# Optimization experiments

Hardware: AMD Instinct MI355X
Metric: run time of the kernel (lower is better)

## Reference

```python
import jax, jax.numpy as jnp
import numpy as np

V = 50257      # vocab size
H = 512        # hidden size
S = 128        # source length
BEAM = 5       # beam width (matches beam_width=5 default)
TMAX = 32      # MAX_LENGTH decode cap
SOS, EOS = 1, 2
NEG = -1e9


def setup_inputs() -> dict:
    key = jax.random.key(0)
    ks = jax.random.split(key, 12)
    p = lambda k, shape: jax.random.normal(k, shape, jnp.float32) * 0.02
    return {
        "input_tokens": jax.random.randint(ks[0], (S,), 0, V),
        "embedding": p(ks[1], (V, H)),
        "enc_Wih": p(ks[2], (3 * H, H)),
        "enc_Whh": p(ks[3], (3 * H, H)),
        "enc_bih": jnp.zeros((3 * H,), jnp.float32),
        "enc_bhh": jnp.zeros((3 * H,), jnp.float32),
        "dec_Wih": p(ks[4], (3 * H, H)),
        "dec_Whh": p(ks[5], (3 * H, H)),
        "dec_bih": jnp.zeros((3 * H,), jnp.float32),
        "dec_bhh": jnp.zeros((3 * H,), jnp.float32),
        "W_concat": p(ks[6], (2 * H, H)),
        "W_vocab": p(ks[7], (H, V)),
    }


def gru_cell(x, h, Wih, Whh, bih, bhh):
    # x, h: [..., H]
    gi = x @ Wih.T + bih
    gh = h @ Whh.T + bhh
    ir, iz, inn = jnp.split(gi, 3, -1)
    hr, hz, hn = jnp.split(gh, 3, -1)
    r = jax.nn.sigmoid(ir + hr)
    z = jax.nn.sigmoid(iz + hz)
    n = jnp.tanh(inn + r * hn)
    return (1.0 - z) * n + z * h


def reference(input_tokens, embedding, enc_Wih, enc_Whh, enc_bih, enc_bhh,
              dec_Wih, dec_Whh, dec_bih, dec_bhh, W_concat, W_vocab):
    # ---- encoder: 1-layer GRU over source tokens ----
    src_emb = embedding[input_tokens]                       # [S, H]

    def enc_step(h, x):
        h2 = gru_cell(x, h, enc_Wih, enc_Whh, enc_bih, enc_bhh)
        return h2, h2

    enc_h, enc_out = jax.lax.scan(enc_step, jnp.zeros((H,), src_emb.dtype), src_emb)
    # enc_out: [S, H], enc_h: [H]

    def decode_step(tokens, hidden):
        # tokens: [B] int, hidden: [B, H]
        x = embedding[tokens]                               # [B, H]
        h = gru_cell(x, hidden, dec_Wih, dec_Whh, dec_bih, dec_bhh)
        attn = jax.nn.softmax(h @ enc_out.T, axis=-1)       # [B, S] Luong dot attention
        ctx = attn @ enc_out                                # [B, H]
        o = jnp.tanh(jnp.concatenate([h, ctx], -1) @ W_concat)
        logp = jax.nn.log_softmax(o @ W_vocab, axis=-1)     # [B, V]
        return logp, h

    # ---- batched beam search (GPU-resident equivalent of the heapq loop) ----
    tokens0 = jnp.full((BEAM,), SOS, jnp.int32)
    hidden0 = jnp.tile(enc_h[None], (BEAM, 1))
    scores0 = jnp.full((BEAM,), NEG, jnp.float32).at[0].set(0.0)
    fin0 = jnp.zeros((BEAM,), bool)
    len0 = jnp.ones((BEAM,), jnp.int32)
    seqs0 = jnp.zeros((BEAM, TMAX), jnp.int32)
    fin_row = jnp.full((V,), NEG, jnp.float32).at[EOS].set(0.0)

    def beam_step(state, t):
        tokens, hidden, scores, finished, lengths, seqs = state
        logp, h2 = decode_step(tokens, hidden)              # [BEAM, V]
        step_lp = jnp.where(finished[:, None], fin_row[None, :], logp)
        cand = scores[:, None] + step_lp                    # [BEAM, V]
        top_scores, flat = jax.lax.top_k(cand.reshape(-1), BEAM)
        parent = flat // V
        tok = (flat % V).astype(jnp.int32)
        par_fin = finished[parent]
        new_fin = par_fin | (tok == EOS)
        new_len = lengths[parent] + jnp.where(par_fin, 0, 1)
        new_seqs = seqs[parent].at[:, t].set(jnp.where(par_fin, 0, tok))
        return (tok, h2[parent], top_scores, new_fin, new_len, new_seqs), None

    state, _ = jax.lax.scan(beam_step, (tokens0, hidden0, scores0, fin0, len0, seqs0),
                            jnp.arange(TMAX))
    _, _, scores, _, lengths, seqs = state
    # length-normalized ranking, matching node.logp / node.leng sort
    norm = scores / lengths.astype(scores.dtype)
    order = jnp.argsort(-norm)
    return seqs[order], norm[order]
```

## Files before the change

### kernel.cpp

```cpp
#include <hip/hip_runtime.h>
#include <cstdint>
#include <cstddef>

#define V_SZ 50257
#define H_SZ 512
#define S_SZ 128
#define NBEAM 5
#define TMAXX 32
#define TOK_SOS 1
#define TOK_EOS 2
#define NEGINF (-1e9f)

#define GW 128
#define NT 512
#define GENC 16
#define COLS_PER_WG 393

#define BI_LEAF(l)  ((l)*32)
#define BI_ROOT     256
#define BI_REL(l)   (512 + (l)*32)
#define BI_ECNT     1024
#define BI_EREL     1056

#define OF_GI    0
#define OF_ENC   196608
#define OF_EW    262144
#define OF_H2    327680
#define OF_AL    332800
#define OF_OTOP  333440
#define OF_PV    336000
#define OF_PM    339200
#define OF_PS    339840
#define OF_SC    340480
#define OI_BASE  340488

template <typename T>
__device__ __forceinline__ T aload(const T* p){
  return __hip_atomic_load((T*)p, __ATOMIC_RELAXED, __HIP_MEMORY_SCOPE_AGENT);
}
template <typename T>
__device__ __forceinline__ void astore(T* p, T v){
  __hip_atomic_store(p, v, __ATOMIC_RELAXED, __HIP_MEMORY_SCOPE_AGENT);
}

__device__ __forceinline__ float wredsum(float a){
#pragma unroll
  for (int m = 32; m; m >>= 1) a += __shfl_xor(a, m, 64);
  return a;
}

template <typename F>
__device__ __forceinline__ void dbar(int* bi, int wid, F&& tail){
  __shared__ int s_last;
  int mygen = 0;
  __syncthreads();
  if (threadIdx.x == 0){
    int leaf = wid >> 4;
    mygen = aload(bi + BI_REL(leaf));
    __builtin_amdgcn_s_waitcnt(0);
    int lo = __hip_atomic_fetch_add(bi + BI_LEAF(leaf), 1, __ATOMIC_RELAXED, __HIP_MEMORY_SCOPE_AGENT);
    int last = 0;
    if (lo == 15){
      astore(bi + BI_LEAF(leaf), 0);
      __builtin_amdgcn_s_waitcnt(0);
      int ro = __hip_atomic_fetch_add(bi + BI_ROOT, 1, __ATOMIC_RELAXED, __HIP_MEMORY_SCOPE_AGENT);
      if (ro == (GW/16) - 1){
        astore(bi + BI_ROOT, 0);
        last = 1;
      }
    }
    if (!last){
      while (aload(bi + BI_REL(leaf)) == mygen) __builtin_amdgcn_s_sleep(4);
    }
    s_last = last;
  }
  __syncthreads();
  if (s_last){
    tail();
    __syncthreads();
    if (threadIdx.x == 0){
      __builtin_amdgcn_s_waitcnt(0);
#pragma unroll
      for (int l = 0; l < GW/16; ++l) astore(bi + BI_REL(l), mygen + 1);
    }
  }
  __syncthreads();
}

__global__ __launch_bounds__(256)
void k_gi(const int* __restrict__ toks, const float* __restrict__ emb,
          const float* __restrict__ eWih, const float* __restrict__ ebih,
          float* __restrict__ ws)
{
  float* fb = ws + 2048;
  float* gi = fb + OF_GI;
  const int tid = threadIdx.x, wid = blockIdx.x, lane = tid & 63, wvi = tid >> 6;
  int Wg = wid*4 + wvi;
  for (int it = 0; it < 192; ++it){
    int idx = Wg*192 + it;
    int s = idx / 1536, j = idx - s*1536;
    const float* er = emb + (size_t)toks[s]*H_SZ;
    const float* wr = eWih + (size_t)j*H_SZ;
    float a = 0.f;
#pragma unroll
    for (int u = 0; u < 8; ++u) a += er[u*64+lane]*wr[u*64+lane];
    a = wredsum(a);
    if (lane == 0) gi[idx] = a + ebih[j];
  }
  if (wid == 0){
    float* sc = fb + OF_SC;
    int* ib = (int*)(fb + OI_BASE);
    if (tid < NBEAM){
      sc[tid] = (tid==0) ? 0.f : NEGINF;
      ib[3200+tid] = TOK_SOS; ib[3208+tid] = 0; ib[3216+tid] = 1; ib[3224+tid] = 0;
    }
    for (int q = tid; q < 2*NBEAM*TMAXX; q += 256) ib[3232+q] = 0;
  }
}

__global__ __launch_bounds__(NT, 1)
void k_enc(const float* __restrict__ eWhh, const float* __restrict__ ebhh,
           float* __restrict__ ws)
{
  int* bi = (int*)ws;
  float* fb = ws + 2048;
  float* gi = fb + OF_GI;
  float* enc = fb + OF_ENC;
  const int tid = threadIdx.x, wid = blockIdx.x, lane = tid & 63, wvi = tid >> 6;
  const int i0 = wid*32;
  __shared__ float smF[96];

  float wreg[12][8];
#pragma unroll
  for (int dd = 0; dd < 12; ++dd){
    int d = wvi*12 + dd, g = d >> 5, il = d & 31;
    const float* wr = eWhh + (size_t)(g*512 + i0 + il)*H_SZ;
#pragma unroll
    for (int u = 0; u < 8; ++u) wreg[dd][u] = wr[u*64+lane];
  }

  for (int s = 0; s < S_SZ; ++s){
    float hreg[8];
    if (s == 0){
#pragma unroll
      for (int u = 0; u < 8; ++u) hreg[u] = 0.f;
    } else {
      const float* hp = enc + (size_t)(s-1)*H_SZ;
#pragma unroll
      for (int u = 0; u < 8; ++u) hreg[u] = aload(hp + u*64 + lane);
    }
#pragma unroll
    for (int dd = 0; dd < 12; ++dd){
      float a = 0.f;
#pragma unroll
      for (int u = 0; u < 8; ++u) a += wreg[dd][u]*hreg[u];
      a = wredsum(a);
      if (lane == 0) smF[wvi*12 + dd] = a;
    }
    __syncthreads();
    if (tid < 32){
      int i = i0 + tid;
      float gr = smF[tid], gz = smF[32+tid], gn = smF[64+tid];
      float gir = gi[s*1536 + i], giz = gi[s*1536 + 512 + i], gin = gi[s*1536 + 1024 + i];
      float hprev = (s==0) ? 0.f : aload(enc + (s-1)*H_SZ + i);
      float r = 1.f/(1.f + expf(-(gir + gr + ebhh[i])));
      float z = 1.f/(1.f + expf(-(giz + gz + ebhh[512+i])));
      float n = tanhf(gin + r*(gn + ebhh[1024+i]));
      astore(enc + s*H_SZ + i, (1.f - z)*n + z*hprev);
    }
    __syncthreads();
    if (tid == 0){
      int g = aload(bi + BI_EREL);
      __builtin_amdgcn_s_waitcnt(0);
      int lo = __hip_atomic_fetch_add(bi + BI_ECNT, 1, __ATOMIC_RELAXED, __HIP_MEMORY_SCOPE_AGENT);
      if (lo == GENC - 1){
        astore(bi + BI_ECNT, 0);
        __builtin_amdgcn_s_waitcnt(0);
        astore(bi + BI_EREL, g + 1);
      } else {
        while (aload(bi + BI_EREL) == g) __builtin_amdgcn_s_sleep(2);
      }
    }
    __syncthreads();
  }
}

__global__ __launch_bounds__(NT)
void k_ew(const float* __restrict__ Wc, float* __restrict__ ws)
{
  float* fb = ws + 2048;
  float* enc = fb + OF_ENC;
  float* EW  = fb + OF_EW;
  const int tid = threadIdx.x, wid = blockIdx.x;
  int jc = wid & 15, sb = wid >> 4;
  int jl = tid & 31, sl = (tid >> 5) & 15;
  int s = sb*16 + sl, j = jc*32 + jl;
  const float* er = enc + (size_t)s*H_SZ;
  const float* wc = Wc + (size_t)512*H_SZ;
  float a = 0.f;
  for (int k = 0; k < 512; ++k) a += er[k]*wc[(size_t)k*H_SZ + j];
  EW[s*H_SZ + j] = a;
}

__global__ __launch_bounds__(NT, 1)
void k_dec(const float* __restrict__ emb,
           const float* __restrict__ dWih, const float* __restrict__ dWhh,
           const float* __restrict__ dbih, const float* __restrict__ dbhh,
           const float* __restrict__ Wc,  const float* __restrict__ Wv,
           float* __restrict__ out, float* __restrict__ ws)
{
  const int wid = blockIdx.x, tid = threadIdx.x;
  const int lane = tid & 63, wvi = tid >> 6;
  int* bi = (int*)ws;
  float* fb = ws + 2048;
  float* enc  = fb + OF_ENC;
  float* EW   = fb + OF_EW;
  float* h2   = fb + OF_H2;
  float* al   = fb + OF_AL;
  float* otop = fb + OF_OTOP;
  float* pv   = fb + OF_PV;
  float* pm   = fb + OF_PM;
  float* ps   = fb + OF_PS;
  float* sc   = fb + OF_SC;
  int* ib   = (int*)(fb + OI_BASE);
  int* pidx = ib;
  int* tokA = ib + 3200;
  int* finA = ib + 3208;
  int* lenA = ib + 3216;
  int* parA = ib + 3224;
  int* seqA = ib + 3232;

  __shared__ float smF[1024];
  __shared__ int   smI[256];
  __shared__ float s_buf[2560];
  __shared__ float s_pp[648];

  for (int t = 0; t < TMAXX; ++t){
    float* h2new = h2 + (t & 1)*2560;
    float* h2old = h2 + ((t & 1) ^ 1)*2560;

    if (tid < NBEAM){ smI[tid] = aload(tokA + tid); smI[8 + tid] = t ? aload(parA + tid) : 0; }
    __syncthreads();
    if (t == 0){
      for (int q = tid; q < 2560; q += NT) s_buf[q] = enc[127*H_SZ + (q & 511)];
    } else {
      for (int q = tid; q < 2560; q += NT){
        int b = q >> 9;
        s_buf[q] = aload(h2old + smI[8 + b]*H_SZ + (q & 511));
      }
    }
    __syncthreads();
    {
      int i0 = wid*4;
      int mat = wvi >> 2;
      float srg[5][8];
      if (mat == 0){
#pragma unroll
        for (int b = 0; b < NBEAM; ++b){
          const float* sp = emb + (size_t)smI[b]*H_SZ;
#pragma unroll
          for (int u = 0; u < 8; ++u) srg[b][u] = sp[u*64+lane];
        }
      } else {
#pragma unroll
        for (int b = 0; b < NBEAM; ++b)
#pragma unroll
          for (int u = 0; u < 8; ++u) srg[b][u] = s_buf[b*512 + u*64 + lane];
      }
      for (int rr = 0; rr < 3; ++rr){
        int R = wvi*3 + rr;
        int rem = R - mat*12;
        int g = rem >> 2, il = rem & 3;
        const float* wr = ((mat==0) ? dWih : dWhh) + (size_t)(g*512 + i0 + il)*H_SZ;
        float wreg[8];
#pragma unroll
        for (int u = 0; u < 8; ++u) wreg[u] = wr[u*64+lane];
#pragma unroll
        for (int b = 0; b < NBEAM; ++b){
          float a = 0.f;
#pragma unroll
          for (int u = 0; u < 8; ++u) a += wreg[u]*srg[b][u];
          a = wredsum(a);
          if (lane == 0) smF[R*5 + b] = a;
        }
      }
      __syncthreads();
      if (tid < 20){
        int b = tid >> 2, il = tid & 3;
        int i = i0 + il;
        float ir  = smF[(0*12 + 0*4 + il)*5 + b] + dbih[i];
        float iz  = smF[(0*12 + 1*4 + il)*5 + b] + dbih[512+i];
        float inn = smF[(0*12 + 2*4 + il)*5 + b] + dbih[1024+i];
        float hr  = smF[(1*12 + 0*4 + il)*5 + b] + dbhh[i];
        float hz  = smF[(1*12 + 1*4 + il)*5 + b] + dbhh[512+i];
        float hn  = smF[(1*12 + 2*4 + il)*5 + b] + dbhh[1024+i];
        float r = 1.f/(1.f + expf(-(ir + hr)));
        float z = 1.f/(1.f + expf(-(iz + hz)));
        float n = tanhf(inn + r*hn);
        float hp = s_buf[b*512 + i];
        astore(h2new + b*H_SZ + i, (1.f - z)*n + z*hp);
      }
    }
    dbar(bi, wid, [&](){});

    for (int q = tid; q < 2560; q += NT) s_buf[q] = aload(h2new + q);
    __syncthreads();
    if (wvi < NBEAM){
      const float* er = enc + (size_t)wid*H_SZ;
      float a = 0.f;
#pragma unroll
      for (int u = 0; u < 8; ++u) a += er[u*64+lane]*s_buf[wvi*512 + u*64 + lane];
      a = wredsum(a);
      if (lane == 0) astore(al + wvi*S_SZ + wid, a);
    }
    if (tid < 320){
      int q = tid % 20, ksl = tid / 20;
      int f = wid*20 + q;
      int b = f >> 9, j = f & 511;
      float a = 0.f;
#pragma unroll 8
      for (int u = 0; u < 32; ++u){
        int k = ksl*32 + u;
        a += s_buf[b*512 + k]*Wc[(size_t)k*H_SZ + j];
      }
      smF[q*16 + ksl] = a;
    }
    __syncthreads();
    if (tid < 20){
      float a = 0.f;
#pragma unroll
      for (int u = 0; u < 16; ++u) a += smF[tid*16 + u];
      astore(otop + wid*20 + tid, a);
    }
    dbar(bi, wid, [&](){});

    if (wvi < NBEAM){
      float a1 = aload(al + wvi*S_SZ + lane), a2 = aload(al + wvi*S_SZ + 64 + lane);
      float m = fmaxf(a1, a2);
#pragma unroll
      for (int mm = 32; mm; mm >>= 1) m = fmaxf(m, __shfl_xor(m, mm, 64));
      float e1 = expf(a1 - m), e2 = expf(a2 - m);
      s_pp[wvi*128 + lane] = e1; s_pp[wvi*128 + 64 + lane] = e2;
      float ssv = wredsum(e1 + e2);
      if (lane == 0) s_pp[640 + wvi] = ssv;
    }
    __syncthreads();
    {
      float acc[5] = {0.f,0.f,0.f,0.f,0.f};
      for (int s2 = 0; s2 < 128; ++s2){
        float e = EW[(size_t)s2*H_SZ + tid];
#pragma unroll
        for (int b = 0; b < NBEAM; ++b) acc[b] += e*s_pp[b*128 + s2];
      }
#pragma unroll
      for (int b = 0; b < NBEAM; ++b)
        s_buf[b*512 + tid] = tanhf(aload(otop + b*512 + tid) + acc[b]/s_pp[640 + b]);
    }
    __syncthreads();
    {
      int vbase = wid*COLS_PER_WG;
      int v = vbase + tid;
      bool act = (tid < COLS_PER_WG) && (v < V_SZ);
      int vc = act ? v : vbase;
      const float* wp = Wv + vc;
      float a0=0.f,a1=0.f,a2=0.f,a3=0.f,a4=0.f;
      for (int hb = 0; hb < H_SZ; hb += 16){
        float wr[16];
#pragma unroll
        for (int u = 0; u < 16; ++u) wr[u] = wp[(size_t)(hb+u)*V_SZ];
#pragma unroll
        for (int u = 0; u < 16; ++u){
          float w = wr[u];
          a0 += w*s_buf[hb+u];
          a1 += w*s_buf[512+hb+u];
          a2 += w*s_buf[1024+hb+u];
          a3 += w*s_buf[1536+hb+u];
          a4 += w*s_buf[2048+hb+u];
        }
      }
      if (!act){ a0=a1=a2=a3=a4=-3e38f; }
      int myv = act ? v : 0x7FFFFFFF;
      float accs[5] = {a0,a1,a2,a3,a4};
#pragma unroll
      for (int b = 0; b < NBEAM; ++b){
        float x = accs[b];
        float m = x;
#pragma unroll
        for (int mm = 32; mm; mm >>= 1) m = fmaxf(m, __shfl_xor(m, mm, 64));
        float e = expf(x - m);
        float ssum = wredsum(e);
        float bv = x; int bc = myv;
        float w5[5]; int i5[5];
#pragma unroll
        for (int r = 0; r < 5; ++r){
          float cv2 = bv; int ci2 = bc;
#pragma unroll
          for (int mm = 32; mm; mm >>= 1){
            float ov = __shfl_xor(cv2, mm, 64); int oi = __shfl_xor(ci2, mm, 64);
            bool take = (ov > cv2) || (ov == cv2 && oi < ci2);
            cv2 = take ? ov : cv2; ci2 = take ? oi : ci2;
          }
          w5[r] = cv2; i5[r] = ci2;
          if (bc == ci2) bv = -3e38f;
        }
        if (lane == 0){
#pragma unroll
          for (int r = 0; r < 5; ++r){ smF[(wvi*5+b)*5+r] = w5[r]; smI[(wvi*5+b)*5+r] = i5[r]; }
          smF[300 + wvi*5 + b] = m;
          smF[360 + wvi*5 + b] = ssum;
        }
      }
      __syncthreads();
      if (tid < NBEAM){
        float M = -3.4e38f, Sv = 0.f;
#pragma unroll
        for (int w8 = 0; w8 < 8; ++w8){
          float m2 = smF[300 + w8*5 + tid], s2 = smF[360 + w8*5 + tid];
          if (m2 > M){ Sv = Sv*expf(M - m2) + s2; M = m2; }
          else       { Sv = Sv + s2*expf(m2 - M); }
        }
        astore(pm + wid*5 + tid, M); astore(ps + wid*5 + tid, Sv);
      }
      if (wvi < NBEAM){
        int b = wvi;
        float cval; int cidx;
        if (lane < 40){ cval = smF[((lane/5)*5 + b)*5 + (lane%5)]; cidx = smI[((lane/5)*5 + b)*5 + (lane%5)]; }
        else { cval = -3e38f; cidx = 0x7FFFFFFF; }
        float bv = cval; int bc = cidx;
#pragma unroll
        for (int r = 0; r < 5; ++r){
          float cv2 = bv; int ci2 = bc;
#pragma unroll
          for (int mm = 32; mm; mm >>= 1){
            float ov = __shfl_xor(cv2, mm, 64); int oi = __shfl_xor(ci2, mm, 64);
            bool take = (ov > cv2) || (ov == cv2 && oi < ci2);
            cv2 = take ? ov : cv2; ci2 = take ? oi : ci2;
          }
          if (lane == 0){ astore(pv + (wid*5+b)*5+r, cv2); astore(pidx + (wid*5+b)*5+r, ci2); }
          if (bc == ci2) bv = -3e38f;
        }
      }
    }
    dbar(bi, wid, [&](){
      int b5 = wvi;
      if (b5 < NBEAM){
        float m1 = aload(pm + lane*5 + b5), s1 = aload(ps + lane*5 + b5);
        float m2 = aload(pm + (64+lane)*5 + b5), s2 = aload(ps + (64+lane)*5 + b5);
        float M, Sv;
        if (m1 >= m2){ M = m1; Sv = s1 + s2*expf(m2 - m1); }
        else         { M = m2; Sv = s2 + s1*expf(m1 - m2); }
#pragma unroll
        for (int mm = 32; mm; mm >>= 1){
          float om = __shfl_xor(M, mm, 64), os = __shfl_xor(Sv, mm, 64);
          if (om > M){ Sv = Sv*expf(M - om) + os; M = om; }
          else       { Sv = Sv + os*expf(om - M); }
        }
        if (lane == 0){ smF[8 + b5] = M; smF[80 + b5] = logf(Sv); }
        float lv[5]; int li[5];
#pragma unroll
        for (int r = 0; r < 5; ++r){ lv[r] = aload(pv + (lane*5 + b5)*5 + r); li[r] = aload(pidx + (lane*5 + b5)*5 + r); }
        for (int r = 0; r < 5; ++r){
          float nv = aload(pv + ((64+lane)*5 + b5)*5 + r); int ni = aload(pidx + ((64+lane)*5 + b5)*5 + r);
          bool ins = (nv > lv[4]) || (nv == lv[4] && ni < li[4]);
          if (!ins) break;
          lv[4] = nv; li[4] = ni;
#pragma unroll
          for (int p = 4; p > 0; --p){
            bool sw = (lv[p] > lv[p-1]) || (lv[p] == lv[p-1] && li[p] < li[p-1]);
            if (sw){ float tv = lv[p]; lv[p] = lv[p-1]; lv[p-1] = tv;
                     int ti = li[p]; li[p] = li[p-1]; li[p-1] = ti; }
          }
        }
        float cv = lv[0]; int ci = li[0];
#pragma unroll
        for (int r = 0; r < 5; ++r){
          float xv = cv; int xi = ci;
#pragma unroll
          for (int mm = 32; mm; mm >>= 1){
            float ov = __shfl_xor(xv, mm, 64); int oi = __shfl_xor(xi, mm, 64);
            bool take = (ov > xv) || (ov == xv && oi < xi);
            xv = take ? ov : xv; xi = take ? oi : xi;
          }
          if (lane == 0){ smF[16 + b5*5 + r] = xv; smI[16 + b5*5 + r] = xi; }
          if (ci == xi){
            lv[0]=lv[1]; li[0]=li[1]; lv[1]=lv[2]; li[1]=li[2];
            lv[2]=lv[3]; li[2]=li[3]; lv[3]=lv[4]; li[3]=li[4];
            lv[4] = -3e38f; li[4] = 0x7FFFFFFF;
            cv = lv[0]; ci = li[0];
          }
        }
      }
      __syncthreads();
      if (wvi == 0){
        float cval = -3e38f; int cflat = 0x7FFFFFFF;
        int b = lane/5, k = lane - b*5;
        if (lane < 25){
          if (aload(finA + b)){
            if (k == 0){ cval = aload(sc + b) + 0.0f; cflat = b*V_SZ + TOK_EOS; }
          } else {
            cval = ((smF[16 + b*5 + k] - smF[8 + b]) - smF[80 + b]) + aload(sc + b);
            cflat = b*V_SZ + smI[16 + b*5 + k];
          }
        }
        float bv = cval; int bc = cflat;
#pragma unroll
        for (int r = 0; r < 5; ++r){
          float xv = bv; int xi = bc;
#pragma unroll
          for (int mm = 32; mm; mm >>= 1){
            float ov = __shfl_xor(xv, mm, 64); int oi = __shfl_xor(xi, mm, 64);
            bool take = (ov > xv) || (ov == xv && oi < xi);
            xv = take ? ov : xv; xi = take ? oi : xi;
          }
          if (lane == 0){ smF[48 + r] = xv; smI[48 + r] = xi; }
          if (bc == xi) bv = -3e38f;
        }
        if (lane < NBEAM){
          int r = lane;
          float nscore = smF[48 + r]; int nfl = smI[48 + r];
          int par = nfl / V_SZ; int tok = nfl - par*V_SZ;
          int ofin = aload(finA + par); int olen = aload(lenA + par);
          int nf = (ofin || tok == TOK_EOS) ? 1 : 0;
          int nl = olen + (ofin ? 0 : 1);
          astore(sc + r, nscore); astore(tokA + r, tok); astore(finA + r, nf);
          astore(lenA + r, nl); astore(parA + r, par);
          smI[56 + r] = par; smI[64 + r] = tok; smI[72 + r] = ofin; smI[80 + r] = nl;
          smF[56 + r] = nscore;
        }
      }
      __syncthreads();
      int cur = t & 1, nxt = 1 - cur;
      if (tid < 160){
        int r = tid >> 5, u = tid & 31;
        int par = smI[56 + r];
        int val = aload(seqA + cur*160 + par*32 + u);
        if (u == t) val = smI[72 + r] ? 0 : smI[64 + r];
        astore(seqA + nxt*160 + r*32 + u, val);
      }
      if (t == TMAXX - 1){
        __syncthreads();
        if (tid == 0){
          float nn[5];
#pragma unroll
          for (int r = 0; r < 5; ++r) nn[r] = smF[56 + r] / (float)smI[80 + r];
          int used = 0;
#pragma unroll
          for (int r = 0; r < 5; ++r){
            int best = -1;
            for (int q2 = 0; q2 < 5; ++q2){
              if (used & (1 << q2)) continue;
              if (best < 0 || nn[q2] > nn[best]) best = q2;
            }
            used |= (1 << best);
            smI[88 + r] = best; smF[64 + r] = nn[best];
          }
        }
        __syncthreads();
        if (tid < 160){
          int r = tid >> 5, u = tid & 31;
          int src = smI[88 + r];
          out[tid] = (float)aload(seqA + nxt*160 + src*32 + u);
        }
        if (tid >= 160 && tid < 165) out[tid] = smF[64 + (tid - 160)];
      }
    });
  }
}

extern "C" void kernel_launch(void* const* d_in, const int* in_sizes, int n_in,
                              void* d_out, int out_size, void* d_ws, size_t ws_size,
                              hipStream_t stream)
{
  (void)in_sizes; (void)n_in; (void)out_size; (void)ws_size;
  hipMemsetAsync(d_ws, 0, 8192, stream);
  float* ws = (float*)d_ws;
  k_gi<<<dim3(256), dim3(256), 0, stream>>>(
      (const int*)d_in[0], (const float*)d_in[1],
      (const float*)d_in[2], (const float*)d_in[4], ws);
  k_enc<<<dim3(GENC), dim3(NT), 0, stream>>>(
      (const float*)d_in[3], (const float*)d_in[5], ws);
  k_ew<<<dim3(128), dim3(NT), 0, stream>>>(
      (const float*)d_in[10], ws);
  k_dec<<<dim3(GW), dim3(NT), 0, stream>>>(
      (const float*)d_in[1],
      (const float*)d_in[6], (const float*)d_in[7],
      (const float*)d_in[8], (const float*)d_in[9],
      (const float*)d_in[10], (const float*)d_in[11],
      (float*)d_out, ws);
}
```

Baseline: 3.673 ms.

## Double decoder workgroups to 256 with split-K vocab projection and register-resident GRU weights

Raises the persistent decoder grid from 128 to 256 workgroups and allows two workgroups per CU. Each group now handles 197 vocab columns and splits the hidden dimension across two halves of the block, combining the halves through shared memory. GRU weight rows are preloaded into registers once, outside the time loop, and the attention and W_concat work and the cross-group top-k and softmax merges are redistributed for the larger grid. This spreads the memory-bound W_vocab streaming over more waves, at the cost of more participants in each grid barrier and an extra shared-memory reduction.

```diff
diff --git a/kernel.cpp b/kernel.cpp
--- a/kernel.cpp
+++ b/kernel.cpp
@@ -11,16 +11,16 @@
 #define TOK_EOS 2
 #define NEGINF (-1e9f)
 
-#define GW 128
+#define GW 256
 #define NT 512
 #define GENC 16
-#define COLS_PER_WG 393
+#define COLS_PER_WG 197
 
 #define BI_LEAF(l)  ((l)*32)
-#define BI_ROOT     256
-#define BI_REL(l)   (512 + (l)*32)
-#define BI_ECNT     1024
-#define BI_EREL     1056
+#define BI_ROOT     544
+#define BI_REL(l)   (1024 + (l)*32)
+#define BI_ECNT     1792
+#define BI_EREL     1824
 
 #define OF_GI    0
 #define OF_ENC   196608
@@ -29,10 +29,15 @@
 #define OF_AL    332800
 #define OF_OTOP  333440
 #define OF_PV    336000
-#define OF_PM    339200
-#define OF_PS    339840
-#define OF_SC    340480
-#define OI_BASE  340488
+#define OF_PM    342400
+#define OF_PS    343680
+#define OF_SC    344960
+#define OI_BASE  344968
+#define I_TOK 6400
+#define I_FIN 6408
+#define I_LEN 6416
+#define I_PAR 6424
+#define I_SEQ 6432
 
 template <typename T>
 __device__ __forceinline__ T aload(const T* p){
@@ -112,9 +117,9 @@
     int* ib = (int*)(fb + OI_BASE);
     if (tid < NBEAM){
       sc[tid] = (tid==0) ? 0.f : NEGINF;
-      ib[3200+tid] = TOK_SOS; ib[3208+tid] = 0; ib[3216+tid] = 1; ib[3224+tid] = 0;
-    }
-    for (int q = tid; q < 2*NBEAM*TMAXX; q += 256) ib[3232+q] = 0;
+      ib[I_TOK+tid] = TOK_SOS; ib[I_FIN+tid] = 0; ib[I_LEN+tid] = 1; ib[I_PAR+tid] = 0;
+    }
+    for (int q = tid; q < 2*NBEAM*TMAXX; q += 256) ib[I_SEQ+q] = 0;
   }
 }
 
@@ -202,7 +207,7 @@
   EW[s*H_SZ + j] = a;
 }
 
-__global__ __launch_bounds__(NT, 1)
+__global__ __launch_bounds__(NT, 2)
 void k_dec(const float* __restrict__ emb,
            const float* __restrict__ dWih, const float* __restrict__ dWhh,
            const float* __restrict__ dbih, const float* __restrict__ dbhh,
@@ -224,16 +229,30 @@
   float* sc   = fb + OF_SC;
   int* ib   = (int*)(fb + OI_BASE);
   int* pidx = ib;
-  int* tokA = ib + 3200;
-  int* finA = ib + 3208;
-  int* lenA = ib + 3216;
-  int* parA = ib + 3224;
-  int* seqA = ib + 3232;
-
-  __shared__ float smF[1024];
+  int* tokA = ib + I_TOK;
+  int* finA = ib + I_FIN;
+  int* lenA = ib + I_LEN;
+  int* parA = ib + I_PAR;
+  int* seqA = ib + I_SEQ;
+
+  __shared__ float smF[1792];
   __shared__ int   smI[256];
   __shared__ float s_buf[2560];
   __shared__ float s_pp[648];
+
+  const int i0 = wid*2;
+  float awreg[2][8];
+  if (wvi < 6){
+#pragma unroll
+    for (int rr = 0; rr < 2; ++rr){
+      int R = wvi*2 + rr;
+      int mat = R / 6, rem = R - mat*6;
+      int g = rem >> 1, il = rem & 1;
+      const float* wr = (mat ? dWhh : dWih) + (size_t)(g*512 + i0 + il)*H_SZ;
+#pragma unroll
+      for (int u = 0; u < 8; ++u) awreg[rr][u] = wr[u*64+lane];
+    }
+  }
 
   for (int t = 0; t < TMAXX; ++t){
     float* h2new = h2 + (t & 1)*2560;
@@ -250,11 +269,9 @@
       }
     }
     __syncthreads();
-    {
-      int i0 = wid*4;
-      int mat = wvi >> 2;
+    if (wvi < 6){
       float srg[5][8];
-      if (mat == 0){
+      if (wvi < 3){
 #pragma unroll
         for (int b = 0; b < NBEAM; ++b){
           const float* sp = emb + (size_t)smI[b]*H_SZ;
@@ -267,55 +284,54 @@
 #pragma unroll
           for (int u = 0; u < 8; ++u) srg[b][u] = s_buf[b*512 + u*64 + lane];
       }
-      for (int rr = 0; rr < 3; ++rr){
-        int R = wvi*3 + rr;
-        int rem = R - mat*12;
-        int g = rem >> 2, il = rem & 3;
-        const float* wr = ((mat==0) ? dWih : dWhh) + (size_t)(g*512 + i0 + il)*H_SZ;
-        float wreg[8];
-#pragma unroll
-        for (int u = 0; u < 8; ++u) wreg[u] = wr[u*64+lane];
+#pragma unroll
+      for (int rr = 0; rr < 2; ++rr){
+        int R = wvi*2 + rr;
 #pragma unroll
         for (int b = 0; b < NBEAM; ++b){
           float a = 0.f;
 #pragma unroll
-          for (int u = 0; u < 8; ++u) a += wreg[u]*srg[b][u];
+          for (int u = 0; u < 8; ++u) a += awreg[rr][u]*srg[b][u];
           a = wredsum(a);
           if (lane == 0) smF[R*5 + b] = a;
         }
       }
-      __syncthreads();
-      if (tid < 20){
-        int b = tid >> 2, il = tid & 3;
-        int i = i0 + il;
-        float ir  = smF[(0*12 + 0*4 + il)*5 + b] + dbih[i];
-        float iz  = smF[(0*12 + 1*4 + il)*5 + b] + dbih[512+i];
-        float inn = smF[(0*12 + 2*4 + il)*5 + b] + dbih[1024+i];
-        float hr  = smF[(1*12 + 0*4 + il)*5 + b] + dbhh[i];
-        float hz  = smF[(1*12 + 1*4 + il)*5 + b] + dbhh[512+i];
-        float hn  = smF[(1*12 + 2*4 + il)*5 + b] + dbhh[1024+i];
-        float r = 1.f/(1.f + expf(-(ir + hr)));
-        float z = 1.f/(1.f + expf(-(iz + hz)));
-        float n = tanhf(inn + r*hn);
-        float hp = s_buf[b*512 + i];
-        astore(h2new + b*H_SZ + i, (1.f - z)*n + z*hp);
-      }
+    }
+    __syncthreads();
+    if (tid < 10){
+      int b = tid >> 1, il = tid & 1;
+      int i = i0 + il;
+      float ir  = smF[(0  + il)*5 + b] + dbih[i];
+      float iz  = smF[(2  + il)*5 + b] + dbih[512+i];
+      float inn = smF[(4  + il)*5 + b] + dbih[1024+i];
+      float hr  = smF[(6  + il)*5 + b] + dbhh[i];
+      float hz  = smF[(8  + il)*5 + b] + dbhh[512+i];
+      float hn  = smF[(10 + il)*5 + b] + dbhh[1024+i];
+      float r = 1.f/(1.f + expf(-(ir + hr)));
+      float z = 1.f/(1.f + expf(-(iz + hz)));
+      float n = tanhf(inn + r*hn);
+      float hp = s_buf[b*512 + i];
+      astore(h2new + b*H_SZ + i, (1.f - z)*n + z*hp);
     }
     dbar(bi, wid, [&](){});
 
     for (int q = tid; q < 2560; q += NT) s_buf[q] = aload(h2new + q);
     __syncthreads();
-    if (wvi < NBEAM){
-      const float* er = enc + (size_t)wid*H_SZ;
-      float a = 0.f;
-#pragma unroll
-      for (int u = 0; u < 8; ++u) a += er[u*64+lane]*s_buf[wvi*512 + u*64 + lane];
-      a = wredsum(a);
-      if (lane == 0) astore(al + wvi*S_SZ + wid, a);
-    }
-    if (tid < 320){
-      int q = tid % 20, ksl = tid / 20;
-      int f = wid*20 + q;
+    if (wvi < 3){
+      int d = wvi*256 + wid;
+      if (d < 640){
+        int b = d >> 7, s = d & 127;
+        const float* er = enc + (size_t)s*H_SZ;
+        float a = 0.f;
+#pragma unroll
+        for (int u = 0; u < 8; ++u) a += er[u*64+lane]*s_buf[b*512 + u*64 + lane];
+        a = wredsum(a);
+        if (lane == 0) astore(al + b*S_SZ + s, a);
+      }
+    }
+    if (tid < 160){
+      int q = tid % 10, ksl = tid / 10;
+      int f = wid*10 + q;
       int b = f >> 9, j = f & 511;
       float a = 0.f;
 #pragma unroll 8
@@ -326,11 +342,11 @@
       smF[q*16 + ksl] = a;
     }
     __syncthreads();
-    if (tid < 20){
+    if (tid < 10){
       float a = 0.f;
 #pragma unroll
       for (int u = 0; u < 16; ++u) a += smF[tid*16 + u];
-      astore(otop + wid*20 + tid, a);
+      astore(otop + wid*10 + tid, a);
     }
     dbar(bi, wid, [&](){});
 
@@ -358,39 +374,90 @@
     }
     __syncthreads();
     {
+      int half = tid >> 8;
+      int c = tid & 255;
       int vbase = wid*COLS_PER_WG;
-      int v = vbase + tid;
-      bool act = (tid < COLS_PER_WG) && (v < V_SZ);
-      int vc = act ? v : vbase;
-      const float* wp = Wv + vc;
+      int vv = vbase + c;
+      bool act = (c < COLS_PER_WG) && (vv < V_SZ);
+      int vc = act ? vv : vbase;
+      const float* wp = Wv + (size_t)(half*256)*V_SZ + vc;
+      const float* ob = s_buf + half*256;
       float a0=0.f,a1=0.f,a2=0.f,a3=0.f,a4=0.f;
-      for (int hb = 0; hb < H_SZ; hb += 16){
-        float wr[16];
-#pragma unroll
-        for (int u = 0; u < 16; ++u) wr[u] = wp[(size_t)(hb+u)*V_SZ];
-#pragma unroll
-        for (int u = 0; u < 16; ++u){
-          float w = wr[u];
-          a0 += w*s_buf[hb+u];
-          a1 += w*s_buf[512+hb+u];
-          a2 += w*s_buf[1024+hb+u];
-          a3 += w*s_buf[1536+hb+u];
-          a4 += w*s_buf[2048+hb+u];
-        }
-      }
-      if (!act){ a0=a1=a2=a3=a4=-3e38f; }
-      int myv = act ? v : 0x7FFFFFFF;
+      for (int hb = 0; hb < 256; hb += 32){
+        float wr[32];
+#pragma unroll
+        for (int u = 0; u < 32; ++u) wr[u] = wp[(size_t)(hb+u)*V_SZ];
+#pragma unroll
+        for (int u = 0; u < 32; ++u){
+          float w = wr[u]; int h = hb + u;
+          a0 += w*ob[h];
+          a1 += w*ob[512+h];
+          a2 += w*ob[1024+h];
+          a3 += w*ob[1536+h];
+          a4 += w*ob[2048+h];
+        }
+      }
       float accs[5] = {a0,a1,a2,a3,a4};
-#pragma unroll
-      for (int b = 0; b < NBEAM; ++b){
-        float x = accs[b];
-        float m = x;
-#pragma unroll
-        for (int mm = 32; mm; mm >>= 1) m = fmaxf(m, __shfl_xor(m, mm, 64));
-        float e = expf(x - m);
-        float ssum = wredsum(e);
-        float bv = x; int bc = myv;
-        float w5[5]; int i5[5];
+      if (half){
+#pragma unroll
+        for (int b = 0; b < NBEAM; ++b) smF[512 + b*256 + c] = accs[b];
+      }
+      __syncthreads();
+      if (!half){
+#pragma unroll
+        for (int b = 0; b < NBEAM; ++b) accs[b] += smF[512 + b*256 + c];
+        if (!act){
+#pragma unroll
+          for (int b = 0; b < NBEAM; ++b) accs[b] = -3e38f;
+        }
+        int myv = act ? vv : 0x7FFFFFFF;
+#pragma unroll
+        for (int b = 0; b < NBEAM; ++b){
+          float x = accs[b];
+          float m = x;
+#pragma unroll
+          for (int mm = 32; mm; mm >>= 1) m = fmaxf(m, __shfl_xor(m, mm, 64));
+          float e = expf(x - m);
+          float ssum = wredsum(e);
+          float bv = x; int bc = myv;
+          float w5[5]; int i5[5];
+#pragma unroll
+          for (int r = 0; r < 5; ++r){
+            float cv2 = bv; int ci2 = bc;
+#pragma unroll
+            for (int mm = 32; mm; mm >>= 1){
+              float ov = __shfl_xor(cv2, mm, 64); int oi = __shfl_xor(ci2, mm, 64);
+              bool take = (ov > cv2) || (ov == cv2 && oi < ci2);
+              cv2 = take ? ov : cv2; ci2 = take ? oi : ci2;
+            }
+            w5[r] = cv2; i5[r] = ci2;
+            if (bc == ci2) bv = -3e38f;
+          }
+          if (lane == 0){
+#pragma unroll
+            for (int r = 0; r < 5; ++r){ smF[(wvi*5+b)*5+r] = w5[r]; smI[(wvi*5+b)*5+r] = i5[r]; }
+            smF[300 + wvi*5 + b] = m;
+            smF[360 + wvi*5 + b] = ssum;
+          }
+        }
+      }
+      __syncthreads();
+      if (tid < NBEAM){
+        float M = -3.4e38f, Sv = 0.f;
+#pragma unroll
+        for (int w8 = 0; w8 < 4; ++w8){
+          float m2 = smF[300 + w8*5 + tid], s2 = smF[360 + w8*5 + tid];
+          if (m2 > M){ Sv = Sv*expf(M - m2) + s2; M = m2; }
+          else       { Sv = Sv + s2*expf(m2 - M); }
+        }
+        astore(pm + wid*5 + tid, M); astore(ps + wid*5 + tid, Sv);
+      }
+      if (wvi < NBEAM){
+        int b = wvi;
+        float cval; int cidx;
+        if (lane < 20){ cval = smF[((lane/5)*5 + b)*5 + (lane%5)]; cidx = smI[((lane/5)*5 + b)*5 + (lane%5)]; }
+        else { cval = -3e38f; cidx = 0x7FFFFFFF; }
+        float bv = cval; int bc = cidx;
 #pragma unroll
         for (int r = 0; r < 5; ++r){
           float cv2 = bv; int ci2 = bc;
@@ -400,42 +467,6 @@
             bool take = (ov > cv2) || (ov == cv2 && oi < ci2);
             cv2 = take ? ov : cv2; ci2 = take ? oi : ci2;
           }
-          w5[r] = cv2; i5[r] = ci2;
-          if (bc == ci2) bv = -3e38f;
-        }
-        if (lane == 0){
-#pragma unroll
-          for (int r = 0; r < 5; ++r){ smF[(wvi*5+b)*5+r] = w5[r]; smI[(wvi*5+b)*5+r] = i5[r]; }
-          smF[300 + wvi*5 + b] = m;
-          smF[360 + wvi*5 + b] = ssum;
-        }
-      }
-      __syncthreads();
-      if (tid < NBEAM){
-        float M = -3.4e38f, Sv = 0.f;
-#pragma unroll
-        for (int w8 = 0; w8 < 8; ++w8){
-          float m2 = smF[300 + w8*5 + tid], s2 = smF[360 + w8*5 + tid];
-          if (m2 > M){ Sv = Sv*expf(M - m2) + s2; M = m2; }
-          else       { Sv = Sv + s2*expf(m2 - M); }
-        }
-        astore(pm + wid*5 + tid, M); astore(ps + wid*5 + tid, Sv);
-      }
-      if (wvi < NBEAM){
-        int b = wvi;
-        float cval; int cidx;
-        if (lane < 40){ cval = smF[((lane/5)*5 + b)*5 + (lane%5)]; cidx = smI[((lane/5)*5 + b)*5 + (lane%5)]; }
-        else { cval = -3e38f; cidx = 0x7FFFFFFF; }
-        float bv = cval; int bc = cidx;
-#pragma unroll
-        for (int r = 0; r < 5; ++r){
-          float cv2 = bv; int ci2 = bc;
-#pragma unroll
-          for (int mm = 32; mm; mm >>= 1){
-            float ov = __shfl_xor(cv2, mm, 64); int oi = __shfl_xor(ci2, mm, 64);
-            bool take = (ov > cv2) || (ov == cv2 && oi < ci2);
-            cv2 = take ? ov : cv2; ci2 = take ? oi : ci2;
-          }
           if (lane == 0){ astore(pv + (wid*5+b)*5+r, cv2); astore(pidx + (wid*5+b)*5+r, ci2); }
           if (bc == ci2) bv = -3e38f;
         }
@@ -444,11 +475,13 @@
     dbar(bi, wid, [&](){
       int b5 = wvi;
       if (b5 < NBEAM){
-        float m1 = aload(pm + lane*5 + b5), s1 = aload(ps + lane*5 + b5);
-        float m2 = aload(pm + (64+lane)*5 + b5), s2 = aload(ps + (64+lane)*5 + b5);
-        float M, Sv;
-        if (m1 >= m2){ M = m1; Sv = s1 + s2*expf(m2 - m1); }
-        else         { M = m2; Sv = s2 + s1*expf(m1 - m2); }
+        float M = aload(pm + lane*5 + b5), Sv = aload(ps + lane*5 + b5);
+#pragma unroll
+        for (int j = 1; j < GW/64; ++j){
+          float m2 = aload(pm + (j*64+lane)*5 + b5), s2 = aload(ps + (j*64+lane)*5 + b5);
+          if (m2 > M){ Sv = Sv*expf(M - m2) + s2; M = m2; }
+          else       { Sv = Sv + s2*expf(m2 - M); }
+        }
 #pragma unroll
         for (int mm = 32; mm; mm >>= 1){
           float om = __shfl_xor(M, mm, 64), os = __shfl_xor(Sv, mm, 64);
@@ -459,16 +492,18 @@
         float lv[5]; int li[5];
 #pragma unroll
         for (int r = 0; r < 5; ++r){ lv[r] = aload(pv + (lane*5 + b5)*5 + r); li[r] = aload(pidx + (lane*5 + b5)*5 + r); }
-        for (int r = 0; r < 5; ++r){
-          float nv = aload(pv + ((64+lane)*5 + b5)*5 + r); int ni = aload(pidx + ((64+lane)*5 + b5)*5 + r);
-          bool ins = (nv > lv[4]) || (nv == lv[4] && ni < li[4]);
-          if (!ins) break;
-          lv[4] = nv; li[4] = ni;
-#pragma unroll
-          for (int p = 4; p > 0; --p){
-            bool sw = (lv[p] > lv[p-1]) || (lv[p] == lv[p-1] && li[p] < li[p-1]);
-            if (sw){ float tv = lv[p]; lv[p] = lv[p-1]; lv[p-1] = tv;
-                     int ti = li[p]; li[p] = li[p-1]; li[p-1] = ti; }
+        for (int j = 1; j < GW/64; ++j){
+          for (int r = 0; r < 5; ++r){
+            float nv = aload(pv + ((j*64+lane)*5 + b5)*5 + r); int ni = aload(pidx + ((j*64+lane)*5 + b5)*5 + r);
+            bool ins = (nv > lv[4]) || (nv == lv[4] && ni < li[4]);
+            if (!ins) break;
+            lv[4] = nv; li[4] = ni;
+#pragma unroll
+            for (int p = 4; p > 0; --p){
+              bool sw = (lv[p] > lv[p-1]) || (lv[p] == lv[p-1] && li[p] < li[p-1]);
+              if (sw){ float tv = lv[p]; lv[p] = lv[p-1]; lv[p-1] = tv;
+                       int ti = li[p]; li[p] = li[p-1]; li[p-1] = ti; }
+            }
           }
         }
         float cv = lv[0]; int ci = li[0];
```

After: 3.935 ms. 1.07x slower.

## Repack vocab projection into padded layout with float4 split-K decoder GEMV

Applied to the files above, without the earlier changes.

Adds a pre-pass that copies W_vocab into a padded, 16-byte-aligned layout in workspace. The decoder then computes logits with float4 loads, four columns per thread, a 4-way split over the hidden dimension reduced through shared memory, and double-buffered register prefetch. It also adds per-wave top-5 and softmax stats, hoists encoder bias loads, batches the merge loads in the barrier tail, and moves workspace offsets. The packing pass reads and writes the whole ~100MB matrix on every call. The new path runs only if the workspace is large enough, falling back to the old path otherwise.

```diff
diff --git a/kernel.cpp b/kernel.cpp
--- a/kernel.cpp
+++ b/kernel.cpp
@@ -16,11 +16,16 @@
 #define GENC 16
 #define COLS_PER_WG 393
 
+#define VPAD 51200
+#define CW4  400
+#define WVP_OFF 1048576
+#define WS_NEED (4194304ull + (size_t)H_SZ*VPAD*4ull)
+
 #define BI_LEAF(l)  ((l)*32)
-#define BI_ROOT     256
-#define BI_REL(l)   (512 + (l)*32)
-#define BI_ECNT     1024
-#define BI_EREL     1056
+#define BI_ROOT     544
+#define BI_REL(l)   (1024 + (l)*32)
+#define BI_ECNT     1792
+#define BI_EREL     1824
 
 #define OF_GI    0
 #define OF_ENC   196608
@@ -29,10 +34,15 @@
 #define OF_AL    332800
 #define OF_OTOP  333440
 #define OF_PV    336000
-#define OF_PM    339200
-#define OF_PS    339840
-#define OF_SC    340480
-#define OI_BASE  340488
+#define OF_PM    342400
+#define OF_PS    343680
+#define OF_SC    344960
+#define OI_BASE  344968
+#define I_TOK 6400
+#define I_FIN 6408
+#define I_LEN 6416
+#define I_PAR 6424
+#define I_SEQ 6432
 
 template <typename T>
 __device__ __forceinline__ T aload(const T* p){
@@ -88,6 +98,22 @@
 }
 
 __global__ __launch_bounds__(256)
+void k_pack(const float* __restrict__ Wv, float* __restrict__ ws)
+{
+  float* wvp = ws + WVP_OFF;
+  const int h  = blockIdx.y;
+  const int v4 = blockIdx.x*256 + threadIdx.x;
+  const int v  = v4*4;
+  const float* src = Wv + (size_t)h*V_SZ;
+  float4 o;
+  o.x = (v+0 < V_SZ) ? src[v+0] : 0.f;
+  o.y = (v+1 < V_SZ) ? src[v+1] : 0.f;
+  o.z = (v+2 < V_SZ) ? src[v+2] : 0.f;
+  o.w = (v+3 < V_SZ) ? src[v+3] : 0.f;
+  *(float4*)(wvp + (size_t)h*VPAD + v) = o;
+}
+
+__global__ __launch_bounds__(256)
 void k_gi(const int* __restrict__ toks, const float* __restrict__ emb,
           const float* __restrict__ eWih, const float* __restrict__ ebih,
           float* __restrict__ ws)
@@ -112,9 +138,9 @@
     int* ib = (int*)(fb + OI_BASE);
     if (tid < NBEAM){
       sc[tid] = (tid==0) ? 0.f : NEGINF;
-      ib[3200+tid] = TOK_SOS; ib[3208+tid] = 0; ib[3216+tid] = 1; ib[3224+tid] = 0;
-    }
-    for (int q = tid; q < 2*NBEAM*TMAXX; q += 256) ib[3232+q] = 0;
+      ib[I_TOK+tid] = TOK_SOS; ib[I_FIN+tid] = 0; ib[I_LEN+tid] = 1; ib[I_PAR+tid] = 0;
+    }
+    for (int q = tid; q < 2*NBEAM*TMAXX; q += 256) ib[I_SEQ+q] = 0;
   }
 }
 
@@ -138,6 +164,11 @@
 #pragma unroll
     for (int u = 0; u < 8; ++u) wreg[dd][u] = wr[u*64+lane];
   }
+  float eb0 = 0.f, eb1 = 0.f, eb2 = 0.f;
+  if (tid < 32){
+    int i = i0 + tid;
+    eb0 = ebhh[i]; eb1 = ebhh[512+i]; eb2 = ebhh[1024+i];
+  }
 
   for (int s = 0; s < S_SZ; ++s){
     float hreg[8];
@@ -163,9 +194,9 @@
       float gr = smF[tid], gz = smF[32+tid], gn = smF[64+tid];
       float gir = gi[s*1536 + i], giz = gi[s*1536 + 512 + i], gin = gi[s*1536 + 1024 + i];
       float hprev = (s==0) ? 0.f : aload(enc + (s-1)*H_SZ + i);
-      float r = 1.f/(1.f + expf(-(gir + gr + ebhh[i])));
-      float z = 1.f/(1.f + expf(-(giz + gz + ebhh[512+i])));
-      float n = tanhf(gin + r*(gn + ebhh[1024+i]));
+      float r = 1.f/(1.f + expf(-(gir + gr + eb0)));
+      float z = 1.f/(1.f + expf(-(giz + gz + eb1)));
+      float n = tanhf(gin + r*(gn + eb2));
       astore(enc + s*H_SZ + i, (1.f - z)*n + z*hprev);
     }
     __syncthreads();
@@ -202,6 +233,7 @@
   EW[s*H_SZ + j] = a;
 }
 
+template<int PACKED>
 __global__ __launch_bounds__(NT, 1)
 void k_dec(const float* __restrict__ emb,
            const float* __restrict__ dWih, const float* __restrict__ dWhh,
@@ -224,16 +256,19 @@
   float* sc   = fb + OF_SC;
   int* ib   = (int*)(fb + OI_BASE);
   int* pidx = ib;
-  int* tokA = ib + 3200;
-  int* finA = ib + 3208;
-  int* lenA = ib + 3216;
-  int* parA = ib + 3224;
-  int* seqA = ib + 3232;
-
-  __shared__ float smF[1024];
+  int* tokA = ib + I_TOK;
+  int* finA = ib + I_FIN;
+  int* lenA = ib + I_LEN;
+  int* parA = ib + I_PAR;
+  int* seqA = ib + I_SEQ;
+
+  __shared__ float smF[512];
   __shared__ int   smI[256];
   __shared__ float s_buf[2560];
   __shared__ float s_pp[648];
+  __shared__ float s_red[PACKED ? 6300 : 4];
+
+  const int i0 = wid*4;
 
   for (int t = 0; t < TMAXX; ++t){
     float* h2new = h2 + (t & 1)*2560;
@@ -251,7 +286,6 @@
     }
     __syncthreads();
     {
-      int i0 = wid*4;
       int mat = wvi >> 2;
       float srg[5][8];
       if (mat == 0){
@@ -357,7 +391,145 @@
         s_buf[b*512 + tid] = tanhf(aload(otop + b*512 + tid) + acc[b]/s_pp[640 + b]);
     }
     __syncthreads();
-    {
+
+    if constexpr (PACKED){
+      const float* wvp = (const float*)(ws + WVP_OFF);
+      const int c4 = tid % 100, slice = tid / 100;
+      float acc[5][4];
+#pragma unroll
+      for (int b = 0; b < 5; ++b)
+#pragma unroll
+        for (int k = 0; k < 4; ++k) acc[b][k] = 0.f;
+      if (tid < 400){
+        const float* wp = wvp + (size_t)(slice*128)*VPAD + wid*CW4 + c4*4;
+        const int hbase = slice*128;
+        float4 bufA[8], bufB[8];
+#pragma unroll
+        for (int u = 0; u < 8; ++u) bufA[u] = *(const float4*)(wp + (size_t)u*VPAD);
+        for (int hb = 0; hb < 128; hb += 16){
+#pragma unroll
+          for (int u = 0; u < 8; ++u) bufB[u] = *(const float4*)(wp + (size_t)(hb+8+u)*VPAD);
+#pragma unroll
+          for (int u = 0; u < 8; ++u){
+            float4 w = bufA[u]; int h = hbase + hb + u;
+#pragma unroll
+            for (int b = 0; b < 5; ++b){
+              float o = s_buf[b*512 + h];
+              acc[b][0] += w.x*o; acc[b][1] += w.y*o; acc[b][2] += w.z*o; acc[b][3] += w.w*o;
+            }
+          }
+          if (hb + 16 < 128){
+#pragma unroll
+            for (int u = 0; u < 8; ++u) bufA[u] = *(const float4*)(wp + (size_t)(hb+16+u)*VPAD);
+          }
+#pragma unroll
+          for (int u = 0; u < 8; ++u){
+            float4 w = bufB[u]; int h = hbase + hb + 8 + u;
+#pragma unroll
+            for (int b = 0; b < 5; ++b){
+              float o = s_buf[b*512 + h];
+              acc[b][0] += w.x*o; acc[b][1] += w.y*o; acc[b][2] += w.z*o; acc[b][3] += w.w*o;
+            }
+          }
+        }
+      }
+      if (tid < 400 && slice > 0){
+        float* rp = s_red + (slice-1)*2100 + c4*21;
+#pragma unroll
+        for (int b = 0; b < 5; ++b)
+#pragma unroll
+          for (int k = 0; k < 4; ++k) rp[b*4+k] = acc[b][k];
+      }
+      __syncthreads();
+      if (wvi < 2){
+        if (tid < 100){
+#pragma unroll
+          for (int s = 0; s < 3; ++s){
+            const float* rp = s_red + s*2100 + tid*21;
+#pragma unroll
+            for (int b = 0; b < 5; ++b)
+#pragma unroll
+              for (int k = 0; k < 4; ++k) acc[b][k] += rp[b*4+k];
+          }
+        }
+        int vb4 = wid*CW4 + tid*4;
+        bool okk[4];
+#pragma unroll
+        for (int k = 0; k < 4; ++k) okk[k] = (tid < 100) && (vb4 + k < V_SZ);
+#pragma unroll
+        for (int b = 0; b < NBEAM; ++b){
+          float x[4]; int id[4];
+#pragma unroll
+          for (int k = 0; k < 4; ++k){
+            x[k]  = okk[k] ? acc[b][k] : -3e38f;
+            id[k] = okk[k] ? vb4 + k   : 0x7FFFFFFF;
+          }
+          float m = fmaxf(fmaxf(x[0],x[1]), fmaxf(x[2],x[3]));
+#pragma unroll
+          for (int mm = 32; mm; mm >>= 1) m = fmaxf(m, __shfl_xor(m, mm, 64));
+          float e = 0.f;
+#pragma unroll
+          for (int k = 0; k < 4; ++k) e += expf(x[k] - m);
+          float ssum = wredsum(e);
+          float w5[5]; int i5[5];
+#pragma unroll
+          for (int r = 0; r < 5; ++r){
+            float bv = x[0]; int bix = id[0];
+#pragma unroll
+            for (int k = 1; k < 4; ++k){
+              bool take = (x[k] > bv) || (x[k] == bv && id[k] < bix);
+              bv = take ? x[k] : bv; bix = take ? id[k] : bix;
+            }
+#pragma unroll
+            for (int mm = 32; mm; mm >>= 1){
+              float ov = __shfl_xor(bv, mm, 64); int oi = __shfl_xor(bix, mm, 64);
+              bool take = (ov > bv) || (ov == bv && oi < bix);
+              bv = take ? ov : bv; bix = take ? oi : bix;
+            }
+            w5[r] = bv; i5[r] = bix;
+#pragma unroll
+            for (int k = 0; k < 4; ++k)
+              if (id[k] == bix){ x[k] = -3e38f; id[k] = 0x7FFFFFFF; }
+          }
+          if (lane == 0){
+#pragma unroll
+            for (int r = 0; r < 5; ++r){ smF[(wvi*5+b)*5+r] = w5[r]; smI[(wvi*5+b)*5+r] = i5[r]; }
+            smF[300 + wvi*5 + b] = m;
+            smF[360 + wvi*5 + b] = ssum;
+          }
+        }
+      }
+      __syncthreads();
+      if (tid < NBEAM){
+        float M = -3.4e38f, Sv = 0.f;
+#pragma unroll
+        for (int w8 = 0; w8 < 2; ++w8){
+          float m2 = smF[300 + w8*5 + tid], s2 = smF[360 + w8*5 + tid];
+          if (m2 > M){ Sv = Sv*expf(M - m2) + s2; M = m2; }
+          else       { Sv = Sv + s2*expf(m2 - M); }
+        }
+        astore(pm + wid*5 + tid, M); astore(ps + wid*5 + tid, Sv);
+      }
+      if (wvi < NBEAM){
+        int b = wvi;
+        float cval; int cidx;
+        if (lane < 10){ cval = smF[((lane/5)*5 + b)*5 + (lane%5)]; cidx = smI[((lane/5)*5 + b)*5 + (lane%5)]; }
+        else { cval = -3e38f; cidx = 0x7FFFFFFF; }
+        float bv = cval; int bc = cidx;
+#pragma unroll
+        for (int r = 0; r < 5; ++r){
+          float cv2 = bv; int ci2 = bc;
+#pragma unroll
+          for (int mm = 32; mm; mm >>= 1){
+            float ov = __shfl_xor(cv2, mm, 64); int oi = __shfl_xor(ci2, mm, 64);
+            bool take = (ov > cv2) || (ov == cv2 && oi < ci2);
+            cv2 = take ? ov : cv2; ci2 = take ? oi : ci2;
+          }
+          if (lane == 0){ astore(pv + (wid*5+b)*5+r, cv2); astore(pidx + (wid*5+b)*5+r, ci2); }
+          if (bc == ci2) bv = -3e38f;
+        }
+      }
+    } else {
       int vbase = wid*COLS_PER_WG;
       int v = vbase + tid;
       bool act = (tid < COLS_PER_WG) && (v < V_SZ);
@@ -441,6 +613,7 @@
         }
       }
     }
+
     dbar(bi, wid, [&](){
       int b5 = wvi;
       if (b5 < NBEAM){
@@ -457,13 +630,16 @@
         }
         if (lane == 0){ smF[8 + b5] = M; smF[80 + b5] = logf(Sv); }
         float lv[5]; int li[5];
-#pragma unroll
-        for (int r = 0; r < 5; ++r){ lv[r] = aload(pv + (lane*5 + b5)*5 + r); li[r] = aload(pidx + (lane*5 + b5)*5 + r); }
+        float nv5[5]; int ni5[5];
+#pragma unroll
         for (int r = 0; r < 5; ++r){
-          float nv = aload(pv + ((64+lane)*5 + b5)*5 + r); int ni = aload(pidx + ((64+lane)*5 + b5)*5 + r);
-          bool ins = (nv > lv[4]) || (nv == lv[4] && ni < li[4]);
+          lv[r]  = aload(pv + (lane*5 + b5)*5 + r);      li[r]  = aload(pidx + (lane*5 + b5)*5 + r);
+          nv5[r] = aload(pv + ((64+lane)*5 + b5)*5 + r); ni5[r] = aload(pidx + ((64+lane)*5 + b5)*5 + r);
+        }
+        for (int r = 0; r < 5; ++r){
+          bool ins = (nv5[r] > lv[4]) || (nv5[r] == lv[4] && ni5[r] < li[4]);
           if (!ins) break;
-          lv[4] = nv; li[4] = ni;
+          lv[4] = nv5[r]; li[4] = ni5[r];
 #pragma unroll
           for (int p = 4; p > 0; --p){
             bool sw = (lv[p] > lv[p-1]) || (lv[p] == lv[p-1] && li[p] < li[p-1]);
@@ -571,9 +747,13 @@
                               void* d_out, int out_size, void* d_ws, size_t ws_size,
                               hipStream_t stream)
 {
-  (void)in_sizes; (void)n_in; (void)out_size; (void)ws_size;
+  (void)in_sizes; (void)n_in; (void)out_size;
   hipMemsetAsync(d_ws, 0, 8192, stream);
   float* ws = (float*)d_ws;
+  const bool packed = ws_size >= (size_t)WS_NEED;
+  if (packed){
+    k_pack<<<dim3(50, 512), dim3(256), 0, stream>>>((const float*)d_in[11], ws);
+  }
   k_gi<<<dim3(256), dim3(256), 0, stream>>>(
       (const int*)d_in[0], (const float*)d_in[1],
       (const float*)d_in[2], (const float*)d_in[4], ws);
@@ -581,10 +761,19 @@
       (const float*)d_in[3], (const float*)d_in[5], ws);
   k_ew<<<dim3(128), dim3(NT), 0, stream>>>(
       (const float*)d_in[10], ws);
-  k_dec<<<dim3(GW), dim3(NT), 0, stream>>>(
-      (const float*)d_in[1],
-      (const float*)d_in[6], (const float*)d_in[7],
-      (const float*)d_in[8], (const float*)d_in[9],
-      (const float*)d_in[10], (const float*)d_in[11],
-      (float*)d_out, ws);
-}
+  if (packed){
+    k_dec<1><<<dim3(GW), dim3(NT), 0, stream>>>(
+        (const float*)d_in[1],
+        (const float*)d_in[6], (const float*)d_in[7],
+        (const float*)d_in[8], (const float*)d_in[9],
+        (const float*)d_in[10], (const float*)d_in[11],
+        (float*)d_out, ws);
+  } else {
+    k_dec<0><<<dim3(GW), dim3(NT), 0, stream>>>(
+        (const float*)d_in[1],
+        (const float*)d_in[6], (const float*)d_in[7],
+        (const float*)d_in[8], (const float*)d_in[9],
+        (const float*)d_in[10], (const float*)d_in[11],
+        (float*)d_out, ws);
+  }
+}
```

Result: slower. 4.329 ms (+17.9%).
